# Optimization experiments

Hardware: AMD Instinct MI355X
Metric: run time of the kernel (lower is better)

Reference implementation:

```python
import jax, jax.numpy as jnp
import numpy as np

EPS = 1e-5
STD = 0.02  # BERT initializer_range


def _bn(x, g, b):
    # BatchNorm1d in training mode: batch stats, biased variance
    m = jnp.mean(x, axis=0)
    v = jnp.mean((x - m) ** 2, axis=0)
    return g * (x - m) / jnp.sqrt(v + EPS) + b


def _gcn(x, src, dst, deg_isqrt, W, b, N):
    norm = deg_isqrt[src] * deg_isqrt[dst]
    msg = (x @ W)[src] * norm[:, None]
    return jax.ops.segment_sum(msg, dst, num_segments=N) + b


def setup_inputs() -> dict:
    key = jax.random.key(0)
    ks = jax.random.split(key, 24)
    B, S, E = 64, 512, 768
    D = E // 2            # 384, embed_size_gnn
    NG = 512              # nodes per graph
    N = B * NG            # 32768 total nodes
    Edges = 1048576
    C = 3                 # num_classes

    inp = {}
    inp["last_h"] = jax.random.normal(ks[0], (B, S, E), jnp.float32)
    inp["first_h"] = jax.random.normal(ks[1], (B, S, E), jnp.float32)
    inp["x_nodes"] = jax.random.normal(ks[2], (N, 300), jnp.float32)
    inp["edge_index"] = jax.random.randint(ks[3], (2, Edges), 0, N, jnp.int32)

    # exactly 2 masked nodes per sample (model reshapes to [B, 2, D])
    rng = np.random.default_rng(0)
    mask = np.zeros((B, NG), np.int32)
    for i in range(B):
        pos = rng.choice(NG, size=2, replace=False)
        mask[i, pos] = 1
    inp["graph_masking"] = jnp.asarray(mask)

    # params (stored [in, out]; torch Linear is [out, in])
    inp["w_pre1"] = STD * jax.random.normal(ks[4], (300, D), jnp.float32)
    inp["b_pre1"] = jnp.zeros((D,), jnp.float32)
    inp["w_pre2"] = STD * jax.random.normal(ks[5], (D, D), jnp.float32)
    inp["b_pre2"] = jnp.zeros((D,), jnp.float32)
    inp["w_conv"] = STD * jax.random.normal(ks[6], (3, D, D), jnp.float32)
    inp["b_conv"] = jnp.zeros((3, D), jnp.float32)
    inp["bng_g"] = jnp.ones((7, D), jnp.float32)
    inp["bng_b"] = jnp.zeros((7, D), jnp.float32)
    inp["w_post1"] = STD * jax.random.normal(ks[7], (D, D), jnp.float32)
    inp["b_post1"] = jnp.zeros((D,), jnp.float32)
    inp["w_post2"] = STD * jax.random.normal(ks[8], (D, D), jnp.float32)
    inp["b_post2"] = jnp.zeros((D,), jnp.float32)
    inp["w_cat"] = STD * jax.random.normal(ks[9], (E, E), jnp.float32)
    inp["b_cat"] = jnp.zeros((E,), jnp.float32)
    inp["bn_g"] = jnp.ones((2, E), jnp.float32)
    inp["bn_b"] = jnp.zeros((2, E), jnp.float32)
    inp["w_out"] = STD * jax.random.normal(ks[10], (E, C), jnp.float32)
    inp["b_out"] = jnp.zeros((C,), jnp.float32)
    return inp


def reference(last_h, first_h, x_nodes, edge_index, graph_masking,
              w_pre1, b_pre1, w_pre2, b_pre2, w_conv, b_conv, bng_g, bng_b,
              w_post1, b_post1, w_post2, b_post2, w_cat, b_cat, bn_g, bn_b,
              w_out, b_out):
    relu = jax.nn.relu
    B, NG = graph_masking.shape
    N = x_nodes.shape[0]

    # sentence branch: first/last hidden-state average, mean pool
    H_sent = jnp.mean(0.5 * (last_h + first_h), axis=1)  # [B, E]

    # GNN pre-MLPs
    x = _bn(relu(x_nodes @ w_pre1 + b_pre1), bng_g[0], bng_b[0])
    x = _bn(relu(x @ w_pre2 + b_pre2), bng_g[1], bng_b[1])

    # self-loop-augmented edge list, degree norm (shared across convs)
    loop = jnp.arange(N, dtype=edge_index.dtype)
    src = jnp.concatenate([edge_index[0], loop])
    dst = jnp.concatenate([edge_index[1], loop])
    deg = jax.ops.segment_sum(jnp.ones_like(dst, jnp.float32), dst, num_segments=N)
    deg_isqrt = jax.lax.rsqrt(deg)

    out = x
    for i in range(3):
        out = _bn(relu(_gcn(x, src, dst, deg_isqrt, w_conv[i], b_conv[i], N)),
                  bng_g[i + 2], bng_b[i + 2])

    out = _bn(relu(out @ w_post1 + b_post1), bng_g[5], bng_b[5])
    out = _bn(relu(out @ w_post2 + b_post2), bng_g[6], bng_b[6])  # [N, D]

    # reshape_graph_embeddings: gather the 2 masked nodes per sample
    # nodes are laid out contiguously per graph (NG nodes each)
    _, sel = jax.lax.top_k(graph_masking, 2)           # [B, 2] local idx, ascending on ties
    gidx = jnp.arange(B)[:, None] * NG + sel            # global node idx
    nodes = out[gidx]                                   # [B, 2, D]
    flat = nodes.reshape(B, -1)                         # [B, E]

    outc = _bn(relu(flat @ w_cat + b_cat), bn_g[0], bn_b[0])
    att = _bn(H_sent, bn_g[1], bn_b[1]) + outc
    return att @ w_out + b_out                          # [B, num_classes]
```

## Files before the change

kernel.cpp:

```cpp
#include <hip/hip_runtime.h>

typedef unsigned int uint32;
typedef unsigned short ushort16;

typedef __attribute__((ext_vector_type(8))) short bf16x8;
typedef __attribute__((ext_vector_type(4))) float f32x4;

#define NNODES 32768
#define DFEAT 384
#define KPAD1 320

__device__ __forceinline__ float bf2f(ushort16 u) {
  union { uint32 i; float f; } x; x.i = ((uint32)u) << 16; return x.f;
}
__device__ __forceinline__ float bflo(uint32 v) {
  union { uint32 i; float f; } x; x.i = v << 16; return x.f;
}
__device__ __forceinline__ float bfhi(uint32 v) {
  union { uint32 i; float f; } x; x.i = v & 0xffff0000u; return x.f;
}
__device__ __forceinline__ ushort16 f2bf(float f) {
  union { float f; uint32 i; } x; x.f = f;
  uint32 r = (x.i + 0x7fffu + ((x.i >> 16) & 1u)) >> 16;
  return (ushort16)r;
}
__device__ __forceinline__ uint32 pack2(float a, float b) {
  return (uint32)f2bf(a) | ((uint32)f2bf(b) << 16);
}

__global__ __launch_bounds__(256) void prep_kernel(
    const float* __restrict__ X, ushort16* __restrict__ A0,
    const int* __restrict__ dst, int* __restrict__ cnt, int E, int degB,
    const float* __restrict__ last, const float* __restrict__ first,
    float* __restrict__ Hpart) {
  int bx = blockIdx.x;
  int tid = threadIdx.x;
  if (bx < 4096) {
    int r = tid >> 5, lane = tid & 31;
    int row = bx * 8 + r;
    const f32x4* xr = (const f32x4*)(X + (size_t)row * 300);
    uint2* ar = (uint2*)(A0 + (size_t)row * KPAD1);
#pragma unroll
    for (int i = 0; i < 3; ++i) {
      int c = lane + i * 32;
      if (c < 75) {
        f32x4 v = xr[c];
        uint2 o; o.x = pack2(v.x, v.y); o.y = pack2(v.z, v.w);
        ar[c] = o;
      } else if (c < 80) {
        uint2 z; z.x = 0u; z.y = 0u;
        ar[c] = z;
      }
    }
  } else if (bx < 4096 + degB) {
    int e = (bx - 4096) * 256 + tid;
    if (e < E) atomicAdd(&cnt[dst[e]], 1);
  } else {
    int idx = bx - 4096 - degB;
    int b = idx & 63, sc = idx >> 6;
    int w = tid >> 6, lane = tid & 63;
    const f32x4* L = (const f32x4*)last;
    const f32x4* F = (const f32x4*)first;
    f32x4 a0 = (f32x4)0.f, a1 = (f32x4)0.f, a2 = (f32x4)0.f;
    size_t rowbase = ((size_t)b * 512 + sc * 32 + w) * 192;
#pragma unroll
    for (int i = 0; i < 8; ++i) {
      size_t rb = rowbase + (size_t)(4 * 192) * i;
      f32x4 l0 = L[rb + lane],       f0 = F[rb + lane];
      f32x4 l1 = L[rb + lane + 64],  f1 = F[rb + lane + 64];
      f32x4 l2 = L[rb + lane + 128], f2 = F[rb + lane + 128];
      a0 += l0 + f0; a1 += l1 + f1; a2 += l2 + f2;
    }
    f32x4* HP = (f32x4*)Hpart;
    size_t p = ((size_t)(sc * 4 + w) * 64 + b) * 192;
    HP[p + lane] = a0; HP[p + lane + 64] = a1; HP[p + lane + 128] = a2;
  }
}

__global__ void scan_kernel(const int* __restrict__ cnt, int* __restrict__ row_start,
                            int* __restrict__ cursor, float* __restrict__ disq) {
  __shared__ int buf[1024];
  int t = threadIdx.x;
  int base = t * 32;
  const int4* c4 = (const int4*)cnt;
  int4 loc[8];
  int s = 0;
#pragma unroll
  for (int i = 0; i < 8; ++i) {
    loc[i] = c4[t * 8 + i];
    s += loc[i].x + loc[i].y + loc[i].z + loc[i].w;
  }
  buf[t] = s; __syncthreads();
  int x = s;
  for (int off = 1; off < 1024; off <<= 1) {
    int v = (t >= off) ? buf[t - off] : 0;
    __syncthreads();
    x += v; buf[t] = x;
    __syncthreads();
  }
  int run = x - s;
#pragma unroll
  for (int i = 0; i < 8; ++i) {
    int4 v = loc[i];
    int j = base + i * 4;
    row_start[j + 0] = run; cursor[j + 0] = run; disq[j + 0] = rsqrtf((float)v.x + 1.0f); run += v.x;
    row_start[j + 1] = run; cursor[j + 1] = run; disq[j + 1] = rsqrtf((float)v.y + 1.0f); run += v.y;
    row_start[j + 2] = run; cursor[j + 2] = run; disq[j + 2] = rsqrtf((float)v.z + 1.0f); run += v.z;
    row_start[j + 3] = run; cursor[j + 3] = run; disq[j + 3] = rsqrtf((float)v.w + 1.0f); run += v.w;
  }
  if (t == 1023) row_start[NNODES] = run;
}

__global__ __launch_bounds__(256) void scatter_kernel(
    const int* __restrict__ src, const int* __restrict__ dst,
    int* __restrict__ cursor, int* __restrict__ csr, int E, int degB,
    const float* __restrict__ Hpart, float* __restrict__ Hsent) {
  int bx = blockIdx.x, t = threadIdx.x;
  if (bx < degB) {
    int e = bx * 256 + t;
    if (e < E) {
      int d = dst[e];
      int pos = atomicAdd(&cursor[d], 1);
      csr[pos] = src[e];
    }
  } else {
    int b = bx - degB;
    if (t < 192) {
      const f32x4* HP = (const f32x4*)Hpart;
      f32x4 h = (f32x4)0.f;
#pragma unroll 4
      for (int p = 0; p < 64; ++p)
        h += HP[((size_t)p * 64 + b) * 192 + t];
      ((f32x4*)Hsent)[(size_t)b * 192 + t] = h * (0.5f / 512.f);
    }
  }
}

__global__ void xform_w_kernel(const float* __restrict__ W, const float* __restrict__ bias,
                               const float* __restrict__ stat, const float* __restrict__ g,
                               const float* __restrict__ bb, float invN,
                               ushort16* __restrict__ BT, float* __restrict__ bias_out,
                               int K, int Kpad, int Nw) {
  __shared__ float red[128];
  int n = blockIdx.x, t = threadIdx.x;
  float part = 0.f;
  for (int k = t; k < Kpad; k += 128) {
    ushort16 o = 0; float contrib = 0.f;
    if (k < K) {
      float ak = 1.f, shk = 0.f;
      if (stat) {
        float s = 0.f, q = 0.f;
        for (int i = 0; i < 8; ++i) { s += stat[k * 8 + i]; q += stat[(DFEAT + k) * 8 + i]; }
        float mean = s * invN, var = q * invN - mean * mean;
        ak = g[k] * rsqrtf(var + 1e-5f);
        shk = bb[k] - ak * mean;
      }
      float w = W[(size_t)k * Nw + n];
      o = f2bf(ak * w);
      contrib = shk * w;
    }
    BT[(size_t)n * Kpad + k] = o;
    part += contrib;
  }
  red[t] = part; __syncthreads();
  for (int off = 64; off > 0; off >>= 1) {
    if (t < off) red[t] += red[t + off];
    __syncthreads();
  }
  if (t == 0) bias_out[n] = (bias ? bias[n] : 0.f) + red[0];
}

#define BM 128
#define BN 128
#define BKT 32
#define LDT 40

template <bool RELU, bool STATS, bool RSCALE>
__global__ __launch_bounds__(256) void gemm_bf16(
    const ushort16* __restrict__ A, int lda, const ushort16* __restrict__ BT, int ldb,
    const float* __restrict__ bias, const float* __restrict__ rowscale,
    ushort16* __restrict__ C, int Ntot, int K, float* __restrict__ stat) {
  __shared__ __attribute__((aligned(16))) ushort16 As[BM * LDT];
  __shared__ __attribute__((aligned(16))) ushort16 Bs[BN * LDT];
  __shared__ float ssum[BN], ssq[BN];
  int bm0 = blockIdx.x * BM, bn0 = blockIdx.y * BN;
  int tid = threadIdx.x;
  if (STATS) {
    if (tid < BN) { ssum[tid] = 0.f; ssq[tid] = 0.f; }
  }
  int lane = tid & 63, wave = tid >> 6;
  int wm = (wave & 1) * 64, wn = (wave >> 1) * 64;
  int l15 = lane & 15, quad = lane >> 4;

  f32x4 acc[4][4];
  for (int i = 0; i < 4; ++i)
    for (int j = 0; j < 4; ++j) acc[i][j] = (f32x4)0.f;

  for (int kk = 0; kk < K; kk += BKT) {
    __syncthreads();
    for (int i = 0; i < 2; ++i) {
      int chunk = tid + i * 256;
      int row = chunk >> 2, cc = chunk & 3;
      uint4 va = *(const uint4*)(A + (size_t)(bm0 + row) * lda + kk + cc * 8);
      *(uint4*)(&As[row * LDT + cc * 8]) = va;
      uint4 vb = *(const uint4*)(BT + (size_t)(bn0 + row) * ldb + kk + cc * 8);
      *(uint4*)(&Bs[row * LDT + cc * 8]) = vb;
    }
    __syncthreads();
    bf16x8 af[4], bfr[4];
    for (int mi = 0; mi < 4; ++mi)
      af[mi] = *(const bf16x8*)(&As[(wm + mi * 16 + l15) * LDT + quad * 8]);
    for (int ni = 0; ni < 4; ++ni)
      bfr[ni] = *(const bf16x8*)(&Bs[(wn + ni * 16 + l15) * LDT + quad * 8]);
    for (int mi = 0; mi < 4; ++mi)
      for (int ni = 0; ni < 4; ++ni)
        acc[mi][ni] = __builtin_amdgcn_mfma_f32_16x16x32_bf16(af[mi], bfr[ni], acc[mi][ni], 0, 0, 0);
  }
  for (int ni = 0; ni < 4; ++ni) {
    int coll = wn + ni * 16 + l15;
    int col = bn0 + coll;
    float bv = bias[col];
    float s = 0.f, q = 0.f;
    for (int mi = 0; mi < 4; ++mi) {
      for (int r = 0; r < 4; ++r) {
        int row = bm0 + wm + mi * 16 + quad * 4 + r;
        float v = acc[mi][ni][r] + bv;
        if (RELU) v = fmaxf(v, 0.f);
        if (RSCALE) v *= rowscale[row];
        C[(size_t)row * Ntot + col] = f2bf(v);
        if (STATS) { s += v; q += v * v; }
      }
    }
    if (STATS) { atomicAdd(&ssum[coll], s); atomicAdd(&ssq[coll], q); }
  }
  if (STATS) {
    __syncthreads();
    int sp = blockIdx.x & 7;
    if (tid < BN) {
      atomicAdd(&stat[(bn0 + tid) * 8 + sp], ssum[tid]);
      atomicAdd(&stat[(DFEAT + bn0 + tid) * 8 + sp], ssq[tid]);
    }
  }
}

__global__ void __launch_bounds__(256) aggregate_kernel(
    const uint32* __restrict__ XWs, const int* __restrict__ csr,
    const int* __restrict__ row_start, const float* __restrict__ disq,
    const float* __restrict__ bconv, uint32* __restrict__ RC2,
    float* __restrict__ stat) {
  int bx = blockIdx.x;
  int unit = (bx & 7) * 768 + (bx >> 3);
  int chunk = unit >> 10;
  int g = unit & 1023;
  __shared__ float ssum[64], ssq[64];
  int tid = threadIdx.x;
  if (tid < 64) { ssum[tid] = 0.f; ssq[tid] = 0.f; }
  __syncthreads();
  int lane = tid & 63, wave = tid >> 6;
  int half = lane >> 5, cl = lane & 31;
  int hb = half << 5;
  int cbase = chunk * 32;
  float b0 = bconv[chunk * 64 + 2 * cl], b1 = bconv[chunk * 64 + 2 * cl + 1];
  float ls0 = 0.f, ls1 = 0.f, lq0 = 0.f, lq1 = 0.f;
  int nodebase = (g * 4 + wave) * 8;
  for (int ni = 0; ni < 8; ++ni) {
    int n = nodebase + ni;
    int beg = row_start[n], end = row_start[n + 1];
    int deg = end - beg;
    int len0 = (deg + 1) >> 1;
    int myBeg = beg + (half ? len0 : 0);
    int myLen = half ? (deg - len0) : len0;
    float a0, a1;
    if (half == 0) {
      uint32 v = XWs[(size_t)n * 192 + cbase + cl];
      a0 = bflo(v); a1 = bfhi(v);
    } else { a0 = 0.f; a1 = 0.f; }
    for (int bb0 = 0; bb0 < len0; bb0 += 32) {
      int rem = myLen - bb0;
      int idx = (cl < rem) ? csr[myBeg + bb0 + cl] : -1;
      int jmax = min(32, len0 - bb0);
      int j = 0;
      for (; j + 8 <= jmax; j += 8) {
        uint32 v[8];
#pragma unroll
        for (int jj = 0; jj < 8; ++jj) {
          int s = __shfl(idx, hb + j + jj, 64);
          int sa = (s < 0) ? 0 : s;
          uint32 m = (s < 0) ? 0u : 0xffffffffu;
          v[jj] = XWs[(size_t)sa * 192 + cbase + cl] & m;
        }
#pragma unroll
        for (int jj = 0; jj < 8; ++jj) { a0 += bflo(v[jj]); a1 += bfhi(v[jj]); }
      }
      for (; j < jmax; ++j) {
        int s = __shfl(idx, hb + j, 64);
        int sa = (s < 0) ? 0 : s;
        uint32 m = (s < 0) ? 0u : 0xffffffffu;
        uint32 v = XWs[(size_t)sa * 192 + cbase + cl] & m;
        a0 += bflo(v); a1 += bfhi(v);
      }
    }
    a0 += __shfl_xor(a0, 32, 64);
    a1 += __shfl_xor(a1, 32, 64);
    if (half == 0) {
      float din = disq[n];
      a0 = fmaxf(din * a0 + b0, 0.f);
      a1 = fmaxf(din * a1 + b1, 0.f);
      RC2[(size_t)n * 192 + cbase + cl] = (uint32)f2bf(a0) | ((uint32)f2bf(a1) << 16);
      ls0 += a0; lq0 += a0 * a0; ls1 += a1; lq1 += a1 * a1;
    }
  }
  if (half == 0) {
    atomicAdd(&ssum[2 * cl], ls0); atomicAdd(&ssum[2 * cl + 1], ls1);
    atomicAdd(&ssq[2 * cl], lq0);  atomicAdd(&ssq[2 * cl + 1], lq1);
  }
  __syncthreads();
  if (tid < 64) {
    int col = chunk * 64 + tid;
    int sp = g & 7;
    atomicAdd(&stat[col * 8 + sp], ssum[tid]);
    atomicAdd(&stat[(DFEAT + col) * 8 + sp], ssq[tid]);
  }
}

__global__ void gather_kernel(const int* __restrict__ mask, const ushort16* __restrict__ R5,
                              const float* __restrict__ stat, const float* __restrict__ g,
                              const float* __restrict__ bb, float invN,
                              float* __restrict__ flat) {
  __shared__ int smin, smax;
  int b = blockIdx.x, t = threadIdx.x;
  if (t == 0) { smin = 1 << 30; smax = -1; }
  __syncthreads();
  for (int p = t; p < 512; p += 384)
    if (mask[b * 512 + p]) { atomicMin(&smin, p); atomicMax(&smax, p); }
  __syncthreads();
  float s = 0.f, q = 0.f;
  for (int i = 0; i < 8; ++i) { s += stat[t * 8 + i]; q += stat[(DFEAT + t) * 8 + i]; }
  float mean = s * invN, var = q * invN - mean * mean;
  float a = g[t] * rsqrtf(var + 1e-5f), sh = bb[t] - a * mean;
  int sel[2] = {smin, smax};
  for (int j = 0; j < 2; ++j) {
    float v = bf2f(R5[(size_t)(b * 512 + sel[j]) * DFEAT + t]);
    flat[(size_t)b * 768 + j * DFEAT + t] = a * v + sh;
  }
}

__global__ void cat_gemm_kernel(const float* __restrict__ flat, const float* __restrict__ Wc,
                                const float* __restrict__ bc, float* __restrict__ out) {
  int t = threadIdx.x;
  int j = blockIdx.x * 64 + (t & 63);
  int b = blockIdx.y * 16 + (t >> 6);
  const float* fr = flat + (size_t)b * 768;
  float acc = bc[j];
#pragma unroll 4
  for (int k = 0; k < 768; ++k) acc += fr[k] * Wc[(size_t)k * 768 + j];
  out[(size_t)b * 768 + j] = fmaxf(acc, 0.f);
}
__global__ void bnstats_kernel(const float* __restrict__ catrelu, const float* __restrict__ Hsent,
                               const float* __restrict__ g, const float* __restrict__ bb,
                               float* __restrict__ aff) {
  int c = blockIdx.x * 64 + threadIdx.x;
  float s1 = 0, q1 = 0, s2 = 0, q2 = 0;
  for (int b = 0; b < 64; ++b) {
    float v = catrelu[b * 768 + c]; s1 += v; q1 += v * v;
    float h = Hsent[b * 768 + c];   s2 += h; q2 += h * h;
  }
  const float inv = 1.0f / 64.0f;
  float m1 = s1 * inv, var1 = q1 * inv - m1 * m1;
  float a1 = g[c] * rsqrtf(var1 + 1e-5f);
  aff[c] = a1; aff[768 + c] = bb[c] - a1 * m1;
  float m2 = s2 * inv, var2 = q2 * inv - m2 * m2;
  float a2 = g[768 + c] * rsqrtf(var2 + 1e-5f);
  aff[1536 + c] = a2; aff[2304 + c] = bb[768 + c] - a2 * m2;
}
__global__ void final_kernel(const float* __restrict__ Hs, const float* __restrict__ catrelu,
                             const float* __restrict__ aff, const float* __restrict__ w_out,
                             const float* __restrict__ b_out, float* __restrict__ out) {
  __shared__ float red[12];
  int b = blockIdx.x, t = threadIdx.x;
  float p0 = 0, p1 = 0, p2 = 0;
  for (int k = t; k < 768; k += 256) {
    float att = (aff[1536 + k] * Hs[b * 768 + k] + aff[2304 + k]) +
                (aff[k] * catrelu[b * 768 + k] + aff[768 + k]);
    p0 += att * w_out[k * 3 + 0];
    p1 += att * w_out[k * 3 + 1];
    p2 += att * w_out[k * 3 + 2];
  }
  for (int off = 32; off > 0; off >>= 1) {
    p0 += __shfl_down(p0, off, 64);
    p1 += __shfl_down(p1, off, 64);
    p2 += __shfl_down(p2, off, 64);
  }
  int wv = t >> 6;
  if ((t & 63) == 0) { red[wv * 3 + 0] = p0; red[wv * 3 + 1] = p1; red[wv * 3 + 2] = p2; }
  __syncthreads();
  if (t == 0) {
    out[b * 3 + 0] = b_out[0] + red[0] + red[3] + red[6] + red[9];
    out[b * 3 + 1] = b_out[1] + red[1] + red[4] + red[7] + red[10];
    out[b * 3 + 2] = b_out[2] + red[2] + red[5] + red[8] + red[11];
  }
}

extern "C" void kernel_launch(void* const* d_in, const int* in_sizes, int n_in,
                              void* d_out, int out_size, void* d_ws, size_t ws_size,
                              hipStream_t stream) {
  const float* last_h  = (const float*)d_in[0];
  const float* first_h = (const float*)d_in[1];
  const float* x_nodes = (const float*)d_in[2];
  const int*   edges   = (const int*)d_in[3];
  const int*   mask    = (const int*)d_in[4];
  const float* w_pre1  = (const float*)d_in[5];
  const float* b_pre1  = (const float*)d_in[6];
  const float* w_pre2  = (const float*)d_in[7];
  const float* b_pre2  = (const float*)d_in[8];
  const float* w_conv  = (const float*)d_in[9];
  const float* b_conv  = (const float*)d_in[10];
  const float* bng_g   = (const float*)d_in[11];
  const float* bng_b   = (const float*)d_in[12];
  const float* w_post1 = (const float*)d_in[13];
  const float* b_post1 = (const float*)d_in[14];
  const float* w_post2 = (const float*)d_in[15];
  const float* b_post2 = (const float*)d_in[16];
  const float* w_cat   = (const float*)d_in[17];
  const float* b_cat   = (const float*)d_in[18];
  const float* bn_g    = (const float*)d_in[19];
  const float* bn_b    = (const float*)d_in[20];
  const float* w_out   = (const float*)d_in[21];
  const float* b_out   = (const float*)d_in[22];
  float* out = (float*)d_out;

  const int E = in_sizes[3] / 2;
  const int* e_src = edges;
  const int* e_dst = edges + E;
  const int degB = (E + 255) / 256;

  char* w = (char*)d_ws;
  size_t off = 0;
  auto alloc = [&](size_t bytes) { size_t p = off; off = (off + bytes + 255) & ~(size_t)255; return p; };
  ushort16* buf0   = (ushort16*)(w + alloc((size_t)NNODES * DFEAT * 2));
  ushort16* buf1   = (ushort16*)(w + alloc((size_t)NNODES * DFEAT * 2));
  int*    csr      = (int*)(w + alloc((size_t)E * 4));
  int*    rowstart = (int*)(w + alloc((size_t)(NNODES + 1) * 4));
  int*    cursor   = (int*)(w + alloc((size_t)NNODES * 4));
  float*  disq     = (float*)(w + alloc((size_t)NNODES * 4));
  ushort16* BT     = (ushort16*)(w + alloc((size_t)DFEAT * DFEAT * 2));
  float*  biasx    = (float*)(w + alloc(DFEAT * 4));
  float*  flat     = (float*)(w + alloc(64 * 768 * 4));
  float*  catrelu  = (float*)(w + alloc(64 * 768 * 4));
  float*  aff64    = (float*)(w + alloc(4 * 768 * 4));
  float*  Hpart    = (float*)(w + alloc((size_t)64 * 64 * 768 * 4));
  float*  Hsent    = (float*)(w + alloc(64 * 768 * 4));
  size_t zoff = off;
  int*   degcnt = (int*)(w + alloc((size_t)NNODES * 4));
  float* stats  = (float*)(w + alloc((size_t)5 * 768 * 8 * 4));
  size_t zbytes = off - zoff;

  hipMemsetAsync(w + zoff, 0, zbytes, stream);

  const float invN = 1.0f / (float)NNODES;
  float* st0 = stats + 0 * 768 * 8;
  float* st1 = stats + 1 * 768 * 8;
  float* st2 = stats + 2 * 768 * 8;
  float* st3 = stats + 3 * 768 * 8;
  float* st4 = stats + 4 * 768 * 8;

  prep_kernel<<<4096 + degB + 1024, 256, 0, stream>>>(x_nodes, buf0, e_dst, degcnt, E, degB,
                                                      last_h, first_h, Hpart);
  xform_w_kernel<<<DFEAT, 128, 0, stream>>>(w_pre1, b_pre1, nullptr, nullptr, nullptr, invN, BT, biasx, 300, KPAD1, DFEAT);
  scan_kernel<<<1, 1024, 0, stream>>>(degcnt, rowstart, cursor, disq);
  scatter_kernel<<<degB + 64, 256, 0, stream>>>(e_src, e_dst, cursor, csr, E, degB, Hpart, Hsent);

  dim3 ggrid(NNODES / BM, DFEAT / BN);

  gemm_bf16<true, true, false><<<ggrid, 256, 0, stream>>>(buf0, KPAD1, BT, KPAD1, biasx, nullptr, buf1, DFEAT, KPAD1, st0);
  xform_w_kernel<<<DFEAT, 128, 0, stream>>>(w_pre2, b_pre2, st0, bng_g + 0 * DFEAT, bng_b + 0 * DFEAT, invN, BT, biasx, DFEAT, DFEAT, DFEAT);

  gemm_bf16<true, true, false><<<ggrid, 256, 0, stream>>>(buf1, DFEAT, BT, DFEAT, biasx, nullptr, buf0, DFEAT, DFEAT, st1);
  xform_w_kernel<<<DFEAT, 128, 0, stream>>>(w_conv + 2 * DFEAT * DFEAT, nullptr, st1, bng_g + 1 * DFEAT, bng_b + 1 * DFEAT, invN, BT, biasx, DFEAT, DFEAT, DFEAT);

  gemm_bf16<false, false, true><<<ggrid, 256, 0, stream>>>(buf0, DFEAT, BT, DFEAT, biasx, disq, buf1, DFEAT, DFEAT, nullptr);

  aggregate_kernel<<<6144, 256, 0, stream>>>((const uint32*)buf1, csr, rowstart, disq, b_conv + 2 * DFEAT, (uint32*)buf0, st2);
  xform_w_kernel<<<DFEAT, 128, 0, stream>>>(w_post1, b_post1, st2, bng_g + 4 * DFEAT, bng_b + 4 * DFEAT, invN, BT, biasx, DFEAT, DFEAT, DFEAT);

  gemm_bf16<true, true, false><<<ggrid, 256, 0, stream>>>(buf0, DFEAT, BT, DFEAT, biasx, nullptr, buf1, DFEAT, DFEAT, st3);
  xform_w_kernel<<<DFEAT, 128, 0, stream>>>(w_post2, b_post2, st3, bng_g + 5 * DFEAT, bng_b + 5 * DFEAT, invN, BT, biasx, DFEAT, DFEAT, DFEAT);

  gemm_bf16<true, true, false><<<ggrid, 256, 0, stream>>>(buf1, DFEAT, BT, DFEAT, biasx, nullptr, buf0, DFEAT, DFEAT, st4);

  gather_kernel<<<64, DFEAT, 0, stream>>>(mask, buf0, st4, bng_g + 6 * DFEAT, bng_b + 6 * DFEAT, invN, flat);
  cat_gemm_kernel<<<dim3(12, 4), 1024, 0, stream>>>(flat, w_cat, b_cat, catrelu);
  bnstats_kernel<<<12, 64, 0, stream>>>(catrelu, Hsent, bn_g, bn_b, aff64);
  final_kernel<<<64, 256, 0, stream>>>(Hsent, catrelu, aff64, w_out, b_out, out);
}
```

Measured before the change: 863.5 us.

## Interleave prep block roles, spread degree atomics, reduce H partials in shared memory

The prep kernel now interleaves its three roles (feature conversion, degree counting, sentence-embedding partial sums) across block indices so each kind of work is spread evenly over the GPU instead of running in sequential phases. Degree atomics are split over 8 sub-counters per node to reduce contention, and the scan kernel sums them. The hidden-state partial sums are first reduced across the four waves in shared memory, which cuts the partial buffer and the later reduction from 64 to 16 slices. In exchange the counter array is eight times larger to zero and read, and the single-block scan does more strided loads.

New measurement: 859.1 us. No clear change (-0.5%).

```diff
diff --git a/kernel.cpp b/kernel.cpp
--- a/kernel.cpp
+++ b/kernel.cpp
@@ -30,14 +30,17 @@
 
 __global__ __launch_bounds__(256) void prep_kernel(
     const float* __restrict__ X, ushort16* __restrict__ A0,
-    const int* __restrict__ dst, int* __restrict__ cnt, int E, int degB,
+    const int* __restrict__ dst, int* __restrict__ cnt8, int E,
     const float* __restrict__ last, const float* __restrict__ first,
     float* __restrict__ Hpart) {
+  __shared__ f32x4 sred[4][192];
   int bx = blockIdx.x;
   int tid = threadIdx.x;
-  if (bx < 4096) {
+  int role = bx % 9, grp = bx / 9;
+  if (role < 4) {
+    int idx = grp * 4 + role;
     int r = tid >> 5, lane = tid & 31;
-    int row = bx * 8 + r;
+    int row = idx * 8 + r;
     const f32x4* xr = (const f32x4*)(X + (size_t)row * 300);
     uint2* ar = (uint2*)(A0 + (size_t)row * KPAD1);
 #pragma unroll
@@ -52,12 +55,13 @@
         ar[c] = z;
       }
     }
-  } else if (bx < 4096 + degB) {
-    int e = (bx - 4096) * 256 + tid;
-    if (e < E) atomicAdd(&cnt[dst[e]], 1);
+  } else if (role < 8) {
+    int idx = grp * 4 + (role - 4);
+    int e = idx * 256 + tid;
+    int sp = bx & 7;
+    if (e < E) atomicAdd(&cnt8[(size_t)dst[e] * 8 + sp], 1);
   } else {
-    int idx = bx - 4096 - degB;
-    int b = idx & 63, sc = idx >> 6;
+    int b = grp & 63, sc = grp >> 6;
     int w = tid >> 6, lane = tid & 63;
     const f32x4* L = (const f32x4*)last;
     const f32x4* F = (const f32x4*)first;
@@ -71,24 +75,29 @@
       f32x4 l2 = L[rb + lane + 128], f2 = F[rb + lane + 128];
       a0 += l0 + f0; a1 += l1 + f1; a2 += l2 + f2;
     }
-    f32x4* HP = (f32x4*)Hpart;
-    size_t p = ((size_t)(sc * 4 + w) * 64 + b) * 192;
-    HP[p + lane] = a0; HP[p + lane + 64] = a1; HP[p + lane + 128] = a2;
-  }
-}
-
-__global__ void scan_kernel(const int* __restrict__ cnt, int* __restrict__ row_start,
+    sred[w][lane] = a0; sred[w][lane + 64] = a1; sred[w][lane + 128] = a2;
+    __syncthreads();
+    if (tid < 192) {
+      f32x4 h = sred[0][tid] + sred[1][tid] + sred[2][tid] + sred[3][tid];
+      ((f32x4*)Hpart)[((size_t)sc * 64 + b) * 192 + tid] = h;
+    }
+  }
+}
+
+__global__ void scan_kernel(const int* __restrict__ cnt8, int* __restrict__ row_start,
                             int* __restrict__ cursor, float* __restrict__ disq) {
   __shared__ int buf[1024];
   int t = threadIdx.x;
   int base = t * 32;
-  const int4* c4 = (const int4*)cnt;
-  int4 loc[8];
+  const int4* c4 = (const int4*)cnt8;
+  int deg[32];
   int s = 0;
 #pragma unroll
-  for (int i = 0; i < 8; ++i) {
-    loc[i] = c4[t * 8 + i];
-    s += loc[i].x + loc[i].y + loc[i].z + loc[i].w;
+  for (int i = 0; i < 32; ++i) {
+    int4 a = c4[(size_t)(base + i) * 2];
+    int4 b = c4[(size_t)(base + i) * 2 + 1];
+    int d = a.x + a.y + a.z + a.w + b.x + b.y + b.z + b.w;
+    deg[i] = d; s += d;
   }
   buf[t] = s; __syncthreads();
   int x = s;
@@ -100,13 +109,11 @@
   }
   int run = x - s;
 #pragma unroll
-  for (int i = 0; i < 8; ++i) {
-    int4 v = loc[i];
-    int j = base + i * 4;
-    row_start[j + 0] = run; cursor[j + 0] = run; disq[j + 0] = rsqrtf((float)v.x + 1.0f); run += v.x;
-    row_start[j + 1] = run; cursor[j + 1] = run; disq[j + 1] = rsqrtf((float)v.y + 1.0f); run += v.y;
-    row_start[j + 2] = run; cursor[j + 2] = run; disq[j + 2] = rsqrtf((float)v.z + 1.0f); run += v.z;
-    row_start[j + 3] = run; cursor[j + 3] = run; disq[j + 3] = rsqrtf((float)v.w + 1.0f); run += v.w;
+  for (int i = 0; i < 32; ++i) {
+    int j = base + i;
+    row_start[j] = run; cursor[j] = run;
+    disq[j] = rsqrtf((float)deg[i] + 1.0f);
+    run += deg[i];
   }
   if (t == 1023) row_start[NNODES] = run;
 }
@@ -128,8 +135,8 @@
     if (t < 192) {
       const f32x4* HP = (const f32x4*)Hpart;
       f32x4 h = (f32x4)0.f;
-#pragma unroll 4
-      for (int p = 0; p < 64; ++p)
+#pragma unroll
+      for (int p = 0; p < 16; ++p)
         h += HP[((size_t)p * 64 + b) * 192 + t];
       ((f32x4*)Hsent)[(size_t)b * 192 + t] = h * (0.5f / 512.f);
     }
@@ -448,11 +455,11 @@
   float*  flat     = (float*)(w + alloc(64 * 768 * 4));
   float*  catrelu  = (float*)(w + alloc(64 * 768 * 4));
   float*  aff64    = (float*)(w + alloc(4 * 768 * 4));
-  float*  Hpart    = (float*)(w + alloc((size_t)64 * 64 * 768 * 4));
+  float*  Hpart    = (float*)(w + alloc((size_t)16 * 64 * 768 * 4));
   float*  Hsent    = (float*)(w + alloc(64 * 768 * 4));
   size_t zoff = off;
-  int*   degcnt = (int*)(w + alloc((size_t)NNODES * 4));
-  float* stats  = (float*)(w + alloc((size_t)5 * 768 * 8 * 4));
+  int*   degcnt8 = (int*)(w + alloc((size_t)NNODES * 8 * 4));
+  float* stats   = (float*)(w + alloc((size_t)5 * 768 * 8 * 4));
   size_t zbytes = off - zoff;
 
   hipMemsetAsync(w + zoff, 0, zbytes, stream);
@@ -464,10 +471,10 @@
   float* st3 = stats + 3 * 768 * 8;
   float* st4 = stats + 4 * 768 * 8;
 
-  prep_kernel<<<4096 + degB + 1024, 256, 0, stream>>>(x_nodes, buf0, e_dst, degcnt, E, degB,
-                                                      last_h, first_h, Hpart);
+  prep_kernel<<<9216, 256, 0, stream>>>(x_nodes, buf0, e_dst, degcnt8, E,
+                                        last_h, first_h, Hpart);
   xform_w_kernel<<<DFEAT, 128, 0, stream>>>(w_pre1, b_pre1, nullptr, nullptr, nullptr, invN, BT, biasx, 300, KPAD1, DFEAT);
-  scan_kernel<<<1, 1024, 0, stream>>>(degcnt, rowstart, cursor, disq);
+  scan_kernel<<<1, 1024, 0, stream>>>(degcnt8, rowstart, cursor, disq);
   scatter_kernel<<<degB + 64, 256, 0, stream>>>(e_src, e_dst, cursor, csr, E, degB, Hpart, Hsent);
 
   dim3 ggrid(NNODES / BM, DFEAT / BN);
```
